# Kernel optimization log

Measured on AMD Instinct MI355X. Metric: run time of the kernel, lower is better.

## Reference

```python
import jax, jax.numpy as jnp
import numpy as np

N_NODES = 50000


def gcn_conv(x, W, b, src, dst, n_nodes):
    """PyG-style GCNConv: self-loops + symmetric deg^-1/2 normalization.

    x: [N, Fin], W: [Fin, Fout], b: [Fout], src/dst: [E] int.
    """
    h = x @ W  # [N, Fout] -- transform before aggregation (small GEMM)
    loop = jnp.arange(n_nodes, dtype=src.dtype)
    src2 = jnp.concatenate([src, loop])  # [E+N]
    dst2 = jnp.concatenate([dst, loop])
    # degree on target nodes (all edge weights = 1, includes self loops)
    deg = jax.ops.segment_sum(jnp.ones(src2.shape[0], dtype=h.dtype), dst2,
                              num_segments=n_nodes)
    dinv = jnp.where(deg > 0, jax.lax.rsqrt(deg), 0.0)
    norm = dinv[src2] * dinv[dst2]  # [E+N]
    msg = h[src2] * norm[:, None]   # gather + scale (memory bound)
    out = jax.ops.segment_sum(msg, dst2, num_segments=n_nodes)  # scatter-add
    return out + b


def setup_inputs() -> dict:
    key = jax.random.key(0)
    ks = jax.random.split(key, 8)
    input_dim, hidden_dim, output_dim = 128, 64, 64
    n_edges = 800000
    x = jax.random.normal(ks[0], (N_NODES, input_dim), dtype=jnp.float32)
    edge_index = jax.random.randint(ks[1], (2, n_edges), 0, N_NODES,
                                    dtype=jnp.int32)
    def glorot(k, fan_in, fan_out):
        s = jnp.sqrt(6.0 / (fan_in + fan_out)).astype(jnp.float32)
        return jax.random.uniform(k, (fan_in, fan_out), jnp.float32, -s, s)
    return {
        "x": x,
        "edge_index": edge_index,
        "W1": glorot(ks[2], input_dim, hidden_dim),
        "b1": jnp.zeros((hidden_dim,), jnp.float32),
        "W2": glorot(ks[3], hidden_dim, output_dim),
        "b2": jnp.zeros((output_dim,), jnp.float32),
        "Wfc": glorot(ks[4], output_dim, 1),
        "bfc": jnp.zeros((1,), jnp.float32),
    }


def reference(x, edge_index, W1, b1, W2, b2, Wfc, bfc):
    src, dst = edge_index[0], edge_index[1]
    h = gcn_conv(x, W1, b1, src, dst, N_NODES)
    h = jax.nn.relu(h)
    h = gcn_conv(h, W2, b2, src, dst, N_NODES)
    logits = h @ Wfc + bfc  # [N, 1]
    return jax.nn.sigmoid(logits)
```

## Files before the change

### kernel.cpp

```cpp
#include <hip/hip_runtime.h>
#include <hip/hip_bf16.h>

#define NN 50000
#define FIN 128
#define NT (NN / 16)
#define NREG 196
#define RCAP 5120
#define SLAB 8960

typedef unsigned short u16;
typedef unsigned int u32;
typedef __attribute__((ext_vector_type(8))) short short8;
typedef __attribute__((ext_vector_type(4))) float floatx4;

__device__ __forceinline__ float b2f(u16 v) {
  union { u32 u; float f; } x; x.u = ((u32)v) << 16; return x.f;
}
__device__ __forceinline__ u16 f2b(float f) {
  union { u32 u; float f; } x; x.f = f;
  u32 r = x.u + 0x7FFFu + ((x.u >> 16) & 1u);
  return (u16)(r >> 16);
}

__global__ __launch_bounds__(256) void k_prep_binA(
    const u32* __restrict__ xw, int nxw, const void* __restrict__ w1, int n1w,
    const void* __restrict__ w2, int n2w, const void* __restrict__ wf, int nfw,
    const u16* __restrict__ b2, const u16* __restrict__ bfc,
    u16* __restrict__ W1h, u16* __restrict__ W1l, float* __restrict__ w2f,
    float* __restrict__ cbias, int* __restrict__ flags,
    const int* __restrict__ src, const int* __restrict__ dst, int E,
    u32* __restrict__ bucket, int* __restrict__ gtail,
    u16* __restrict__ g, float* __restrict__ tvec) {
  int t = threadIdx.x;
  int blk = blockIdx.x;
  if (blk >= 33) {
    __shared__ int hist[NREG];
    __shared__ int base[NREG];
    for (int i = t; i < NREG; i += 256) hist[i] = 0;
    __syncthreads();
    int sl = blk - 33, nsl = 256;
    int lo = (int)((long long)sl * E / nsl);
    int hi = (int)((long long)(sl + 1) * E / nsl);
    for (int e = lo + t; e < hi; e += 256) atomicAdd(&hist[dst[e] >> 8], 1);
    __syncthreads();
    for (int i = t; i < NREG; i += 256) {
      int c = hist[i];
      base[i] = (c > 0) ? atomicAdd(&gtail[i], c) : 0;
      hist[i] = 0;
    }
    __syncthreads();
    for (int e = lo + t; e < hi; e += 256) {
      int d = dst[e];
      int r = d >> 8;
      int ofs = base[r] + atomicAdd(&hist[r], 1);
      if (ofs < RCAP)
        bucket[(size_t)r * RCAP + ofs] = ((u32)(d & 255) << 16) | (u32)src[e];
    }
    return;
  }
  __shared__ int sc[2];
  if (t < 2) sc[t] = 0;
  __syncthreads();
  if (blk < 32) {
    const u32* p = (const u32*)w1;
    int samples = n1w < 1024 ? n1w : 1024;
    int score = 0;
    for (int i = t; i < samples; i += 256) {
      u32 w = p[i];
      u32 e = (w >> 7) & 0xFFu;
      score += (e >= 100u && e <= 132u) ? 1 : -1;
    }
    if (score) atomicAdd(&sc[0], score);
    if (blk == 0) {
      int sn = nxw < 1024 ? nxw : 1024;
      int sx = 0;
      for (int i = t; i < sn; i += 256) {
        u32 w = xw[i];
        u32 e = (w >> 7) & 0xFFu;
        sx += (e >= 100u && e <= 132u) ? 1 : -1;
      }
      if (sx) atomicAdd(&sc[1], sx);
    }
    __syncthreads();
    int f1 = sc[0] > 0;
    if (blk == 0 && t == 0) {
      flags[0] = sc[1] > 0;
      flags[1] = f1;
    }
    int i = blk * 256 + t;
    int j = i & 7, L = (i >> 3) & 63, f = i >> 9;
    int k = (f >> 2) * 32 + (L >> 4) * 8 + j;
    int n = (f & 3) * 16 + (L & 15);
    int idx = k * 64 + n;
    float v = f1 ? b2f(((const u16*)w1)[idx]) : ((const float*)w1)[idx];
    u16 hb = f2b(v);
    W1h[i] = hb;
    W1l[i] = f2b(v - b2f(hb));
  } else {
    const u32* p2 = (const u32*)w2;
    const u32* pf = (const u32*)wf;
    int n2s = n2w < 1024 ? n2w : 1024;
    int nfs = nfw < 1024 ? nfw : 1024;
    int s2 = 0, sf = 0;
    for (int i = t; i < n2s; i += 256) {
      u32 w = p2[i];
      u32 e = (w >> 7) & 0xFFu;
      s2 += (e >= 100u && e <= 132u) ? 1 : -1;
    }
    for (int i = t; i < nfs; i += 256) {
      u32 w = pf[i];
      u32 e = (w >> 7) & 0xFFu;
      sf += (e >= 100u && e <= 132u) ? 1 : -1;
    }
    if (s2) atomicAdd(&sc[0], s2);
    if (sf) atomicAdd(&sc[1], sf);
    __syncthreads();
    int f2 = sc[0] > 0, f3 = sc[1] > 0;
    if (t == 0) { flags[2] = f2; flags[3] = f3; }
    if (t < 64) {
      float acc = 0.f;
      for (int j = 0; j < 64; ++j) {
        float w2v = f2 ? b2f(((const u16*)w2)[t * 64 + j])
                       : ((const float*)w2)[t * 64 + j];
        float wfv = f3 ? b2f(((const u16*)wf)[j]) : ((const float*)wf)[j];
        acc += w2v * wfv;
      }
      w2f[t] = acc;
    } else if (t == 64) {
      float acc = b2f(bfc[0]);
      for (int j = 0; j < 64; ++j) {
        float wfv = f3 ? b2f(((const u16*)wf)[j]) : ((const float*)wf)[j];
        acc += b2f(b2[j]) * wfv;
      }
      cbias[0] = acc;
    } else if (t >= 128 && t < 192) {
      g[(size_t)NN * 64 + (t - 128)] = 0;
    } else if (t == 192) {
      tvec[NN] = 0.f;
    }
  }
}

__global__ __launch_bounds__(256) void k_binB1(const u32* __restrict__ bucket,
                                               const int* __restrict__ gtail,
                                               int* __restrict__ cnt,
                                               int* __restrict__ rowstart,
                                               float* __restrict__ dinv) {
  __shared__ int h[256];
  __shared__ int smem[4];
  int r = blockIdx.x, t = threadIdx.x;
  h[t] = 0;
  __syncthreads();
  int n = gtail[r];
  if (n > RCAP) n = RCAP;
  const u32* b = bucket + (size_t)r * RCAP;
  for (int i = t; i < n; i += 256) atomicAdd(&h[b[i] >> 16], 1);
  __syncthreads();
  int v = r * 256 + t;
  int c = (v < NN) ? h[t] : 0;
  if (v < NN) {
    cnt[v] = c;
    dinv[v] = rsqrtf((float)(c + 1));
  }
  int p = (c + 15) & ~15;
  int lane = t & 63, w = t >> 6;
  int xv = p;
  for (int d = 1; d < 64; d <<= 1) {
    int y = __shfl_up(xv, d);
    if (lane >= d) xv += y;
  }
  if (lane == 63) smem[w] = xv;
  __syncthreads();
  int add = 0;
  for (int j = 0; j < w; ++j) add += smem[j];
  xv += add;
  if (v < NN) rowstart[v] = r * SLAB + xv - p;
}

__global__ __launch_bounds__(256) void k_gemm_scatter(
    const u32* __restrict__ bucket, const int* __restrict__ gtail,
    const int* __restrict__ rowstart, const int* __restrict__ cnt,
    u16* __restrict__ csr,
    const void* __restrict__ X, const u16* __restrict__ Wh,
    const u16* __restrict__ Wl, const float* __restrict__ dinv,
    u16* __restrict__ g, const int* __restrict__ flags) {
  int t = threadIdx.x;
  if (blockIdx.x < NREG) {
    __shared__ int off[256];
    int r = blockIdx.x;
    int v = r * 256 + t;
    int grs = (v < NN) ? rowstart[v] : 0;
    off[t] = grs;
    __syncthreads();
    int n = gtail[r];
    if (n > RCAP) n = RCAP;
    const u32* b = bucket + (size_t)r * RCAP;
    for (int i = t; i < n; i += 256) {
      u32 p = b[i];
      int pos = atomicAdd(&off[p >> 16], 1);
      csr[pos] = (u16)(p & 0xFFFFu);
    }
    __syncthreads();
    if (v < NN) {
      int end = grs + ((cnt[v] + 15) & ~15);
      for (int pos = off[t]; pos < end; ++pos) csr[pos] = (u16)NN;
    }
    return;
  }
  constexpr int KC = FIN / 32;
  int wave = t >> 6, lane = t & 63;
  int rt = (blockIdx.x - NREG) * 4 + wave;
  if (rt >= NT) return;
  int m = rt * 16 + (lane & 15);
  int q = (lane >> 4) * 8;
  bool xb = flags[0] != 0;

  short8 ah[KC], al[KC];
  if (xb) {
    const u16* xr = (const u16*)X + (size_t)m * FIN + q;
#pragma unroll
    for (int kc = 0; kc < KC; ++kc) ah[kc] = *(const short8*)(xr + kc * 32);
  } else {
    const float* xr = (const float*)X + (size_t)m * FIN + q;
#pragma unroll
    for (int kc = 0; kc < KC; ++kc) {
      float4 v0 = *(const float4*)(xr + kc * 32);
      float4 v1 = *(const float4*)(xr + kc * 32 + 4);
      float v[8] = {v0.x, v0.y, v0.z, v0.w, v1.x, v1.y, v1.z, v1.w};
      short8 h8, l8;
#pragma unroll
      for (int j = 0; j < 8; ++j) {
        u16 hb = f2b(v[j]);
        h8[j] = (short)hb;
        l8[j] = (short)f2b(v[j] - b2f(hb));
      }
      ah[kc] = h8;
      al[kc] = l8;
    }
  }

  int row0 = rt * 16 + (lane >> 4) * 4;
  int c0 = lane & 15;
  float dvr[4];
#pragma unroll
  for (int r = 0; r < 4; ++r) dvr[r] = dinv[row0 + r];
#pragma unroll
  for (int ct = 0; ct < 4; ++ct) {
    short8 bh[KC], bl[KC];
#pragma unroll
    for (int kc = 0; kc < KC; ++kc) {
      size_t fo = ((size_t)((kc * 4 + ct) * 64 + lane)) * 8;
      bh[kc] = *(const short8*)(Wh + fo);
      bl[kc] = *(const short8*)(Wl + fo);
    }
    floatx4 acc = (floatx4)(0.f);
#pragma unroll
    for (int kc = 0; kc < KC; ++kc) {
      if (!xb)
        acc = __builtin_amdgcn_mfma_f32_16x16x32_bf16(al[kc], bh[kc], acc, 0, 0, 0);
      acc = __builtin_amdgcn_mfma_f32_16x16x32_bf16(ah[kc], bl[kc], acc, 0, 0, 0);
      acc = __builtin_amdgcn_mfma_f32_16x16x32_bf16(ah[kc], bh[kc], acc, 0, 0, 0);
    }
    size_t o = (size_t)row0 * 64 + ct * 16 + c0;
#pragma unroll
    for (int r = 0; r < 4; ++r) g[o + (size_t)r * 64] = f2b(acc[r] * dvr[r]);
  }
}

__global__ __launch_bounds__(256) void k_agg1t(const u16* __restrict__ g,
                                               const float* __restrict__ dinv,
                                               const int* __restrict__ rowstart,
                                               const int* __restrict__ cnt,
                                               const u16* __restrict__ csr,
                                               const u16* __restrict__ bias,
                                               const float* __restrict__ w2f,
                                               float* __restrict__ tvec) {
  int tid = threadIdx.x;
  int wave = tid >> 6, lane = tid & 63;
  int v = (blockIdx.x * 4 + wave) * 4;
  int rs[4], pd[4];
  float dvl[4], acc[4];
  int pm = 0;
#pragma unroll
  for (int n = 0; n < 4; ++n) {
    rs[n] = rowstart[v + n];
    pd[n] = (cnt[v + n] + 15) & ~15;
    dvl[n] = dinv[v + n];
    acc[n] = b2f(g[(size_t)(v + n) * 64 + lane]);
    pm = pd[n] > pm ? pd[n] : pm;
  }
  for (int j = 0; j < pm; j += 16) {
    u32 cw[4][8];
    bool act[4];
#pragma unroll
    for (int n = 0; n < 4; ++n) {
      act[n] = j < pd[n];
      if (act[n]) {
        int b = rs[n] + j;
        uint4 c0 = *(const uint4*)(csr + b);
        uint4 c1 = *(const uint4*)(csr + b + 8);
        cw[n][0] = c0.x; cw[n][1] = c0.y; cw[n][2] = c0.z; cw[n][3] = c0.w;
        cw[n][4] = c1.x; cw[n][5] = c1.y; cw[n][6] = c1.z; cw[n][7] = c1.w;
      }
    }
    float hh[4][16];
#pragma unroll
    for (int n = 0; n < 4; ++n) {
      if (act[n]) {
#pragma unroll
        for (int i = 0; i < 8; ++i) {
          hh[n][2 * i] = b2f(g[(size_t)(cw[n][i] & 0xFFFFu) * 64 + lane]);
          hh[n][2 * i + 1] = b2f(g[(size_t)(cw[n][i] >> 16) * 64 + lane]);
        }
      }
    }
#pragma unroll
    for (int n = 0; n < 4; ++n) {
      if (act[n]) {
        float s0 = (hh[n][0] + hh[n][1]) + (hh[n][2] + hh[n][3]);
        float s1 = (hh[n][4] + hh[n][5]) + (hh[n][6] + hh[n][7]);
        float s2 = (hh[n][8] + hh[n][9]) + (hh[n][10] + hh[n][11]);
        float s3 = (hh[n][12] + hh[n][13]) + (hh[n][14] + hh[n][15]);
        acc[n] += (s0 + s1) + (s2 + s3);
      }
    }
  }
  float bv = b2f(bias[lane]);
  float wfv = w2f[lane];
  float val[4];
#pragma unroll
  for (int n = 0; n < 4; ++n) {
    val[n] = fmaxf(dvl[n] * acc[n] + bv, 0.0f) * wfv;
    for (int o = 32; o > 0; o >>= 1) val[n] += __shfl_xor(val[n], o);
  }
#pragma unroll
  for (int n = 0; n < 4; ++n)
    if (lane == n) tvec[v + n] = dvl[n] * val[n];
}

__global__ __launch_bounds__(256) void k_aggz(const float* __restrict__ tvec,
                                              const float* __restrict__ dinv,
                                              const int* __restrict__ rowstart,
                                              const int* __restrict__ cnt,
                                              const u16* __restrict__ csr,
                                              const float* __restrict__ cbias,
                                              void* __restrict__ out,
                                              const int* __restrict__ flags) {
  int tid = threadIdx.x;
  int wave = tid >> 6, lane = tid & 63;
  int sub = lane >> 4, slot = lane & 15;
  int v = blockIdx.x * 16 + wave * 4 + sub;
  int rs = rowstart[v];
  int pdeg = (cnt[v] + 15) & ~15;
  float acc = 0.f;
  for (int j = slot; j < pdeg; j += 16) acc += tvec[csr[rs + j]];
  for (int o = 8; o > 0; o >>= 1) acc += __shfl_xor(acc, o);
  if (slot == 0) {
    float dv = dinv[v];
    float z = dv * (acc + tvec[v]) + cbias[0];
    float sg = 1.0f / (1.0f + __expf(-z));
    if (flags[0]) ((u16*)out)[v] = f2b(sg);
    else ((float*)out)[v] = sg;
  }
}

extern "C" void kernel_launch(void* const* d_in, const int* in_sizes, int n_in,
                              void* d_out, int out_size, void* d_ws, size_t ws_size,
                              hipStream_t stream) {
  const void* x = d_in[0];
  const int* ei = (const int*)d_in[1];
  const void* W1 = d_in[2];
  const u16* b1 = (const u16*)d_in[3];
  const void* W2 = d_in[4];
  const u16* b2 = (const u16*)d_in[5];
  const void* Wfc = d_in[6];
  const u16* bfc = (const u16*)d_in[7];

  int E = in_sizes[1] / 2;
  const int* src = ei;
  const int* dst = ei + E;

  char* base = (char*)d_ws;
  size_t off = 0;
  auto alloc = [&](size_t bytes) {
    void* p = base + off;
    off = (off + bytes + 255) & ~(size_t)255;
    return p;
  };
  int* flags = (int*)alloc(8 * 4);
  u16* W1h = (u16*)alloc((size_t)FIN * 64 * 2);
  u16* W1l = (u16*)alloc((size_t)FIN * 64 * 2);
  float* w2f = (float*)alloc(64 * 4);
  float* cbias = (float*)alloc(4);
  int* cnt = (int*)alloc((size_t)NN * 4);
  int* rowstart = (int*)alloc((size_t)NN * 4);
  int* gtail = (int*)alloc((size_t)NREG * 4);
  u32* bucket = (u32*)alloc((size_t)NREG * RCAP * 4);
  u16* csr = (u16*)alloc((size_t)NREG * SLAB * 2);
  float* dinv = (float*)alloc((size_t)NN * 4);
  u16* g = (u16*)alloc((size_t)(NN + 1) * 64 * 2);
  float* tvec = (float*)alloc((size_t)(NN + 1) * 4);

  hipMemsetAsync(gtail, 0, (size_t)NREG * 4, stream);
  k_prep_binA<<<289, 256, 0, stream>>>(
      (const u32*)x, in_sizes[0] / 2, W1, in_sizes[2] / 2, W2, in_sizes[4] / 2,
      Wfc, in_sizes[6] / 2, b2, bfc, W1h, W1l, w2f, cbias, flags, src, dst, E,
      bucket, gtail, g, tvec);
  k_binB1<<<NREG, 256, 0, stream>>>(bucket, gtail, cnt, rowstart, dinv);
  k_gemm_scatter<<<NREG + (NT + 3) / 4, 256, 0, stream>>>(
      bucket, gtail, rowstart, cnt, csr, x, W1h, W1l, dinv, g, flags);
  k_agg1t<<<NN / 16, 256, 0, stream>>>(g, dinv, rowstart, cnt, csr, b1, w2f,
                                       tvec);
  k_aggz<<<NN / 16, 256, 0, stream>>>(tvec, dinv, rowstart, cnt, csr, cbias,
                                      d_out, flags);
}
```

Before: 159.6 us.

## Split layer-1 features into two 32-column halves, drop binB1 kernel, inline dinv

```diff
diff --git a/kernel.cpp b/kernel.cpp
--- a/kernel.cpp
+++ b/kernel.cpp
@@ -7,6 +7,7 @@
 #define NREG 196
 #define RCAP 5120
 #define SLAB 8960
+#define NB_AGG ((NN + 31) / 32)
 
 typedef unsigned short u16;
 typedef unsigned int u32;
@@ -29,8 +30,8 @@
     u16* __restrict__ W1h, u16* __restrict__ W1l, float* __restrict__ w2f,
     float* __restrict__ cbias, int* __restrict__ flags,
     const int* __restrict__ src, const int* __restrict__ dst, int E,
-    u32* __restrict__ bucket, int* __restrict__ gtail,
-    u16* __restrict__ g, float* __restrict__ tvec) {
+    u32* __restrict__ bucket, int* __restrict__ gtail, int* __restrict__ cnt,
+    u16* __restrict__ g0, u16* __restrict__ g1, float* __restrict__ tvec) {
   int t = threadIdx.x;
   int blk = blockIdx.x;
   if (blk >= 33) {
@@ -41,7 +42,11 @@
     int sl = blk - 33, nsl = 256;
     int lo = (int)((long long)sl * E / nsl);
     int hi = (int)((long long)(sl + 1) * E / nsl);
-    for (int e = lo + t; e < hi; e += 256) atomicAdd(&hist[dst[e] >> 8], 1);
+    for (int e = lo + t; e < hi; e += 256) {
+      int d = dst[e];
+      atomicAdd(&hist[d >> 8], 1);
+      atomicAdd(&cnt[d], 1);
+    }
     __syncthreads();
     for (int i = t; i < NREG; i += 256) {
       int c = hist[i];
@@ -133,76 +138,57 @@
         acc += b2f(b2[j]) * wfv;
       }
       cbias[0] = acc;
-    } else if (t >= 128 && t < 192) {
-      g[(size_t)NN * 64 + (t - 128)] = 0;
+    } else if (t >= 128 && t < 160) {
+      g0[(size_t)NN * 32 + (t - 128)] = 0;
+    } else if (t >= 160 && t < 192) {
+      g1[(size_t)NN * 32 + (t - 160)] = 0;
     } else if (t == 192) {
       tvec[NN] = 0.f;
     }
   }
 }
 
-__global__ __launch_bounds__(256) void k_binB1(const u32* __restrict__ bucket,
-                                               const int* __restrict__ gtail,
-                                               int* __restrict__ cnt,
-                                               int* __restrict__ rowstart,
-                                               float* __restrict__ dinv) {
-  __shared__ int h[256];
-  __shared__ int smem[4];
-  int r = blockIdx.x, t = threadIdx.x;
-  h[t] = 0;
-  __syncthreads();
-  int n = gtail[r];
-  if (n > RCAP) n = RCAP;
-  const u32* b = bucket + (size_t)r * RCAP;
-  for (int i = t; i < n; i += 256) atomicAdd(&h[b[i] >> 16], 1);
-  __syncthreads();
-  int v = r * 256 + t;
-  int c = (v < NN) ? h[t] : 0;
-  if (v < NN) {
-    cnt[v] = c;
-    dinv[v] = rsqrtf((float)(c + 1));
-  }
-  int p = (c + 15) & ~15;
-  int lane = t & 63, w = t >> 6;
-  int xv = p;
-  for (int d = 1; d < 64; d <<= 1) {
-    int y = __shfl_up(xv, d);
-    if (lane >= d) xv += y;
-  }
-  if (lane == 63) smem[w] = xv;
-  __syncthreads();
-  int add = 0;
-  for (int j = 0; j < w; ++j) add += smem[j];
-  xv += add;
-  if (v < NN) rowstart[v] = r * SLAB + xv - p;
-}
-
 __global__ __launch_bounds__(256) void k_gemm_scatter(
     const u32* __restrict__ bucket, const int* __restrict__ gtail,
-    const int* __restrict__ rowstart, const int* __restrict__ cnt,
+    int* __restrict__ rowstart, const int* __restrict__ cnt,
     u16* __restrict__ csr,
     const void* __restrict__ X, const u16* __restrict__ Wh,
-    const u16* __restrict__ Wl, const float* __restrict__ dinv,
-    u16* __restrict__ g, const int* __restrict__ flags) {
+    const u16* __restrict__ Wl, u16* __restrict__ g0, u16* __restrict__ g1,
+    const int* __restrict__ flags) {
   int t = threadIdx.x;
   if (blockIdx.x < NREG) {
     __shared__ int off[256];
+    __shared__ int sm4[4];
     int r = blockIdx.x;
     int v = r * 256 + t;
-    int grs = (v < NN) ? rowstart[v] : 0;
+    int c = (v < NN) ? cnt[v] : 0;
+    int p = (c + 15) & ~15;
+    int lane = t & 63, w = t >> 6;
+    int xv = p;
+    for (int d = 1; d < 64; d <<= 1) {
+      int y = __shfl_up(xv, d);
+      if (lane >= d) xv += y;
+    }
+    if (lane == 63) sm4[w] = xv;
+    __syncthreads();
+    int add = 0;
+    for (int j2 = 0; j2 < w; ++j2) add += sm4[j2];
+    xv += add;
+    int grs = r * SLAB + xv - p;
+    if (v < NN) rowstart[v] = grs;
     off[t] = grs;
     __syncthreads();
     int n = gtail[r];
     if (n > RCAP) n = RCAP;
     const u32* b = bucket + (size_t)r * RCAP;
     for (int i = t; i < n; i += 256) {
-      u32 p = b[i];
-      int pos = atomicAdd(&off[p >> 16], 1);
-      csr[pos] = (u16)(p & 0xFFFFu);
+      u32 pk = b[i];
+      int pos = atomicAdd(&off[pk >> 16], 1);
+      csr[pos] = (u16)(pk & 0xFFFFu);
     }
     __syncthreads();
     if (v < NN) {
-      int end = grs + ((cnt[v] + 15) & ~15);
+      int end = grs + p;
       for (int pos = off[t]; pos < end; ++pos) csr[pos] = (u16)NN;
     }
     return;
@@ -243,7 +229,8 @@
   int c0 = lane & 15;
   float dvr[4];
 #pragma unroll
-  for (int r = 0; r < 4; ++r) dvr[r] = dinv[row0 + r];
+  for (int r = 0; r < 4; ++r)
+    dvr[r] = rsqrtf((float)(cnt[row0 + r] + 1));
 #pragma unroll
   for (int ct = 0; ct < 4; ++ct) {
     short8 bh[KC], bl[KC];
@@ -261,32 +248,43 @@
       acc = __builtin_amdgcn_mfma_f32_16x16x32_bf16(ah[kc], bl[kc], acc, 0, 0, 0);
       acc = __builtin_amdgcn_mfma_f32_16x16x32_bf16(ah[kc], bh[kc], acc, 0, 0, 0);
     }
-    size_t o = (size_t)row0 * 64 + ct * 16 + c0;
-#pragma unroll
-    for (int r = 0; r < 4; ++r) g[o + (size_t)r * 64] = f2b(acc[r] * dvr[r]);
-  }
-}
-
-__global__ __launch_bounds__(256) void k_agg1t(const u16* __restrict__ g,
-                                               const float* __restrict__ dinv,
+#pragma unroll
+    for (int r = 0; r < 4; ++r) {
+      u16 ov = f2b(acc[r] * dvr[r]);
+      if (ct < 2)
+        g0[(size_t)(row0 + r) * 32 + ct * 16 + c0] = ov;
+      else
+        g1[(size_t)(row0 + r) * 32 + (ct - 2) * 16 + c0] = ov;
+    }
+  }
+}
+
+__global__ __launch_bounds__(256) void k_agg1p(const u16* __restrict__ gp,
                                                const int* __restrict__ rowstart,
                                                const int* __restrict__ cnt,
                                                const u16* __restrict__ csr,
                                                const u16* __restrict__ bias,
                                                const float* __restrict__ w2f,
-                                               float* __restrict__ tvec) {
+                                               float* __restrict__ tvec,
+                                               int pass) {
   int tid = threadIdx.x;
   int wave = tid >> 6, lane = tid & 63;
-  int v = (blockIdx.x * 4 + wave) * 4;
+  int h = lane >> 5, col = lane & 31;
+  int vb = (blockIdx.x * 4 + wave) * 8 + h * 4;
   int rs[4], pd[4];
   float dvl[4], acc[4];
+  bool ok[4];
   int pm = 0;
 #pragma unroll
   for (int n = 0; n < 4; ++n) {
-    rs[n] = rowstart[v + n];
-    pd[n] = (cnt[v + n] + 15) & ~15;
-    dvl[n] = dinv[v + n];
-    acc[n] = b2f(g[(size_t)(v + n) * 64 + lane]);
+    int nv = vb + n;
+    ok[n] = nv < NN;
+    int cv = ok[n] ? nv : 0;
+    int c = ok[n] ? cnt[cv] : 0;
+    rs[n] = rowstart[cv];
+    pd[n] = ok[n] ? ((c + 15) & ~15) : 0;
+    dvl[n] = rsqrtf((float)(c + 1));
+    acc[n] = ok[n] ? b2f(gp[(size_t)cv * 32 + col]) : 0.f;
     pm = pd[n] > pm ? pd[n] : pm;
   }
   for (int j = 0; j < pm; j += 16) {
@@ -297,10 +295,10 @@
       act[n] = j < pd[n];
       if (act[n]) {
         int b = rs[n] + j;
-        uint4 c0 = *(const uint4*)(csr + b);
-        uint4 c1 = *(const uint4*)(csr + b + 8);
-        cw[n][0] = c0.x; cw[n][1] = c0.y; cw[n][2] = c0.z; cw[n][3] = c0.w;
-        cw[n][4] = c1.x; cw[n][5] = c1.y; cw[n][6] = c1.z; cw[n][7] = c1.w;
+        uint4 uq0 = *(const uint4*)(csr + b);
+        uint4 uq1 = *(const uint4*)(csr + b + 8);
+        cw[n][0] = uq0.x; cw[n][1] = uq0.y; cw[n][2] = uq0.z; cw[n][3] = uq0.w;
+        cw[n][4] = uq1.x; cw[n][5] = uq1.y; cw[n][6] = uq1.z; cw[n][7] = uq1.w;
       }
     }
     float hh[4][16];
@@ -309,8 +307,8 @@
       if (act[n]) {
 #pragma unroll
         for (int i = 0; i < 8; ++i) {
-          hh[n][2 * i] = b2f(g[(size_t)(cw[n][i] & 0xFFFFu) * 64 + lane]);
-          hh[n][2 * i + 1] = b2f(g[(size_t)(cw[n][i] >> 16) * 64 + lane]);
+          hh[n][2 * i] = b2f(gp[(size_t)(cw[n][i] & 0xFFFFu) * 32 + col]);
+          hh[n][2 * i + 1] = b2f(gp[(size_t)(cw[n][i] >> 16) * 32 + col]);
         }
       }
     }
@@ -325,21 +323,22 @@
       }
     }
   }
-  float bv = b2f(bias[lane]);
-  float wfv = w2f[lane];
-  float val[4];
+  int c = col + pass * 32;
+  float bv = b2f(bias[c]);
+  float wfv = w2f[c];
 #pragma unroll
   for (int n = 0; n < 4; ++n) {
-    val[n] = fmaxf(dvl[n] * acc[n] + bv, 0.0f) * wfv;
-    for (int o = 32; o > 0; o >>= 1) val[n] += __shfl_xor(val[n], o);
-  }
-#pragma unroll
-  for (int n = 0; n < 4; ++n)
-    if (lane == n) tvec[v + n] = dvl[n] * val[n];
+    float val = fmaxf(dvl[n] * acc[n] + bv, 0.0f) * wfv;
+    for (int o = 16; o > 0; o >>= 1) val += __shfl_xor(val, o);
+    if (col == n && ok[n]) {
+      int nv = vb + n;
+      float rr = dvl[n] * val;
+      tvec[nv] = pass ? (tvec[nv] + rr) : rr;
+    }
+  }
 }
 
 __global__ __launch_bounds__(256) void k_aggz(const float* __restrict__ tvec,
-                                              const float* __restrict__ dinv,
                                               const int* __restrict__ rowstart,
                                               const int* __restrict__ cnt,
                                               const u16* __restrict__ csr,
@@ -351,12 +350,13 @@
   int sub = lane >> 4, slot = lane & 15;
   int v = blockIdx.x * 16 + wave * 4 + sub;
   int rs = rowstart[v];
-  int pdeg = (cnt[v] + 15) & ~15;
+  int cv = cnt[v];
+  int pdeg = (cv + 15) & ~15;
   float acc = 0.f;
   for (int j = slot; j < pdeg; j += 16) acc += tvec[csr[rs + j]];
   for (int o = 8; o > 0; o >>= 1) acc += __shfl_xor(acc, o);
   if (slot == 0) {
-    float dv = dinv[v];
+    float dv = rsqrtf((float)(cv + 1));
     float z = dv * (acc + tvec[v]) + cbias[0];
     float sg = 1.0f / (1.0f + __expf(-z));
     if (flags[0]) ((u16*)out)[v] = f2b(sg);
@@ -392,25 +392,25 @@
   u16* W1l = (u16*)alloc((size_t)FIN * 64 * 2);
   float* w2f = (float*)alloc(64 * 4);
   float* cbias = (float*)alloc(4);
-  int* cnt = (int*)alloc((size_t)NN * 4);
   int* rowstart = (int*)alloc((size_t)NN * 4);
   int* gtail = (int*)alloc((size_t)NREG * 4);
+  int* cnt = (int*)alloc((size_t)NN * 4);
   u32* bucket = (u32*)alloc((size_t)NREG * RCAP * 4);
   u16* csr = (u16*)alloc((size_t)NREG * SLAB * 2);
-  float* dinv = (float*)alloc((size_t)NN * 4);
-  u16* g = (u16*)alloc((size_t)(NN + 1) * 64 * 2);
+  u16* g0 = (u16*)alloc((size_t)(NN + 1) * 32 * 2);
+  u16* g1 = (u16*)alloc((size_t)(NN + 1) * 32 * 2);
   float* tvec = (float*)alloc((size_t)(NN + 1) * 4);
 
-  hipMemsetAsync(gtail, 0, (size_t)NREG * 4, stream);
+  size_t zbytes = (size_t)((char*)(cnt + NN) - (char*)gtail);
+  hipMemsetAsync(gtail, 0, zbytes, stream);
   k_prep_binA<<<289, 256, 0, stream>>>(
       (const u32*)x, in_sizes[0] / 2, W1, in_sizes[2] / 2, W2, in_sizes[4] / 2,
       Wfc, in_sizes[6] / 2, b2, bfc, W1h, W1l, w2f, cbias, flags, src, dst, E,
-      bucket, gtail, g, tvec);
-  k_binB1<<<NREG, 256, 0, stream>>>(bucket, gtail, cnt, rowstart, dinv);
+      bucket, gtail, cnt, g0, g1, tvec);
   k_gemm_scatter<<<NREG + (NT + 3) / 4, 256, 0, stream>>>(
-      bucket, gtail, rowstart, cnt, csr, x, W1h, W1l, dinv, g, flags);
-  k_agg1t<<<NN / 16, 256, 0, stream>>>(g, dinv, rowstart, cnt, csr, b1, w2f,
-                                       tvec);
-  k_aggz<<<NN / 16, 256, 0, stream>>>(tvec, dinv, rowstart, cnt, csr, cbias,
-                                      d_out, flags);
-}
+      bucket, gtail, rowstart, cnt, csr, x, W1h, W1l, g0, g1, flags);
+  k_agg1p<<<NB_AGG, 256, 0, stream>>>(g0, rowstart, cnt, csr, b1, w2f, tvec, 0);
+  k_agg1p<<<NB_AGG, 256, 0, stream>>>(g1, rowstart, cnt, csr, b1, w2f, tvec, 1);
+  k_aggz<<<NN / 16, 256, 0, stream>>>(tvec, rowstart, cnt, csr, cbias, d_out,
+                                      flags);
+}
```

Measured after the change: 193.1 us. 1.21x slower.

## Build CSR via global atomic degree count and direct scatter, dropping bucket pass

Applied to the files above, without the earlier changes.

```diff
diff --git a/kernel.cpp b/kernel.cpp
--- a/kernel.cpp
+++ b/kernel.cpp
@@ -5,8 +5,10 @@
 #define FIN 128
 #define NT (NN / 16)
 #define NREG 196
-#define RCAP 5120
 #define SLAB 8960
+#define NSLH 512
+#define NSLS 512
+#define NGEMB ((NT + 3) / 4)
 
 typedef unsigned short u16;
 typedef unsigned int u32;
@@ -22,40 +24,21 @@
   return (u16)(r >> 16);
 }
 
-__global__ __launch_bounds__(256) void k_prep_binA(
+__global__ __launch_bounds__(256) void k_prep_hist(
     const u32* __restrict__ xw, int nxw, const void* __restrict__ w1, int n1w,
     const void* __restrict__ w2, int n2w, const void* __restrict__ wf, int nfw,
     const u16* __restrict__ b2, const u16* __restrict__ bfc,
     u16* __restrict__ W1h, u16* __restrict__ W1l, float* __restrict__ w2f,
     float* __restrict__ cbias, int* __restrict__ flags,
-    const int* __restrict__ src, const int* __restrict__ dst, int E,
-    u32* __restrict__ bucket, int* __restrict__ gtail,
+    const int* __restrict__ dst, int E, int* __restrict__ cnt,
     u16* __restrict__ g, float* __restrict__ tvec) {
   int t = threadIdx.x;
   int blk = blockIdx.x;
   if (blk >= 33) {
-    __shared__ int hist[NREG];
-    __shared__ int base[NREG];
-    for (int i = t; i < NREG; i += 256) hist[i] = 0;
-    __syncthreads();
-    int sl = blk - 33, nsl = 256;
-    int lo = (int)((long long)sl * E / nsl);
-    int hi = (int)((long long)(sl + 1) * E / nsl);
-    for (int e = lo + t; e < hi; e += 256) atomicAdd(&hist[dst[e] >> 8], 1);
-    __syncthreads();
-    for (int i = t; i < NREG; i += 256) {
-      int c = hist[i];
-      base[i] = (c > 0) ? atomicAdd(&gtail[i], c) : 0;
-      hist[i] = 0;
-    }
-    __syncthreads();
-    for (int e = lo + t; e < hi; e += 256) {
-      int d = dst[e];
-      int r = d >> 8;
-      int ofs = base[r] + atomicAdd(&hist[r], 1);
-      if (ofs < RCAP)
-        bucket[(size_t)r * RCAP + ofs] = ((u32)(d & 255) << 16) | (u32)src[e];
-    }
+    int sl = blk - 33;
+    int lo = (int)((long long)sl * E / NSLH);
+    int hi = (int)((long long)(sl + 1) * E / NSLH);
+    for (int e = lo + t; e < hi; e += 256) atomicAdd(&cnt[dst[e]], 1);
     return;
   }
   __shared__ int sc[2];
@@ -141,27 +124,14 @@
   }
 }
 
-__global__ __launch_bounds__(256) void k_binB1(const u32* __restrict__ bucket,
-                                               const int* __restrict__ gtail,
-                                               int* __restrict__ cnt,
-                                               int* __restrict__ rowstart,
-                                               float* __restrict__ dinv) {
-  __shared__ int h[256];
-  __shared__ int smem[4];
+__global__ __launch_bounds__(256) void k_scan(const int* __restrict__ cnt,
+                                              int* __restrict__ rowstart,
+                                              int* __restrict__ wo,
+                                              u16* __restrict__ csr) {
+  __shared__ int sm4[4];
   int r = blockIdx.x, t = threadIdx.x;
-  h[t] = 0;
-  __syncthreads();
-  int n = gtail[r];
-  if (n > RCAP) n = RCAP;
-  const u32* b = bucket + (size_t)r * RCAP;
-  for (int i = t; i < n; i += 256) atomicAdd(&h[b[i] >> 16], 1);
-  __syncthreads();
   int v = r * 256 + t;
-  int c = (v < NN) ? h[t] : 0;
-  if (v < NN) {
-    cnt[v] = c;
-    dinv[v] = rsqrtf((float)(c + 1));
-  }
+  int c = (v < NN) ? cnt[v] : 0;
   int p = (c + 15) & ~15;
   int lane = t & 63, w = t >> 6;
   int xv = p;
@@ -169,47 +139,41 @@
     int y = __shfl_up(xv, d);
     if (lane >= d) xv += y;
   }
-  if (lane == 63) smem[w] = xv;
+  if (lane == 63) sm4[w] = xv;
   __syncthreads();
   int add = 0;
-  for (int j = 0; j < w; ++j) add += smem[j];
+  for (int j = 0; j < w; ++j) add += sm4[j];
   xv += add;
-  if (v < NN) rowstart[v] = r * SLAB + xv - p;
+  int grs = r * SLAB + xv - p;
+  if (v < NN) {
+    rowstart[v] = grs;
+    wo[v] = grs;
+    for (int pos = grs + c; pos < grs + p; ++pos) csr[pos] = (u16)NN;
+  }
 }
 
 __global__ __launch_bounds__(256) void k_gemm_scatter(
-    const u32* __restrict__ bucket, const int* __restrict__ gtail,
-    const int* __restrict__ rowstart, const int* __restrict__ cnt,
-    u16* __restrict__ csr,
+    const int* __restrict__ src, const int* __restrict__ dst, int E,
+    int* __restrict__ wo, u16* __restrict__ csr,
     const void* __restrict__ X, const u16* __restrict__ Wh,
-    const u16* __restrict__ Wl, const float* __restrict__ dinv,
+    const u16* __restrict__ Wl, const int* __restrict__ cnt,
     u16* __restrict__ g, const int* __restrict__ flags) {
   int t = threadIdx.x;
-  if (blockIdx.x < NREG) {
-    __shared__ int off[256];
-    int r = blockIdx.x;
-    int v = r * 256 + t;
-    int grs = (v < NN) ? rowstart[v] : 0;
-    off[t] = grs;
-    __syncthreads();
-    int n = gtail[r];
-    if (n > RCAP) n = RCAP;
-    const u32* b = bucket + (size_t)r * RCAP;
-    for (int i = t; i < n; i += 256) {
-      u32 p = b[i];
-      int pos = atomicAdd(&off[p >> 16], 1);
-      csr[pos] = (u16)(p & 0xFFFFu);
-    }
-    __syncthreads();
-    if (v < NN) {
-      int end = grs + ((cnt[v] + 15) & ~15);
-      for (int pos = off[t]; pos < end; ++pos) csr[pos] = (u16)NN;
+  if (blockIdx.x >= NGEMB) {
+    int sl = blockIdx.x - NGEMB;
+    int lo = (int)((long long)sl * E / NSLS);
+    int hi = (int)((long long)(sl + 1) * E / NSLS);
+    for (int e = lo + t; e < hi; e += 256) {
+      int d = dst[e];
+      int s = src[e];
+      int pos = atomicAdd(&wo[d], 1);
+      csr[pos] = (u16)s;
     }
     return;
   }
   constexpr int KC = FIN / 32;
   int wave = t >> 6, lane = t & 63;
-  int rt = (blockIdx.x - NREG) * 4 + wave;
+  int rt = blockIdx.x * 4 + wave;
   if (rt >= NT) return;
   int m = rt * 16 + (lane & 15);
   int q = (lane >> 4) * 8;
@@ -243,7 +207,8 @@
   int c0 = lane & 15;
   float dvr[4];
 #pragma unroll
-  for (int r = 0; r < 4; ++r) dvr[r] = dinv[row0 + r];
+  for (int r = 0; r < 4; ++r)
+    dvr[r] = rsqrtf((float)(cnt[row0 + r] + 1));
 #pragma unroll
   for (int ct = 0; ct < 4; ++ct) {
     short8 bh[KC], bl[KC];
@@ -268,9 +233,8 @@
 }
 
 __global__ __launch_bounds__(256) void k_agg1t(const u16* __restrict__ g,
-                                               const float* __restrict__ dinv,
+                                               const int* __restrict__ cnt,
                                                const int* __restrict__ rowstart,
-                                               const int* __restrict__ cnt,
                                                const u16* __restrict__ csr,
                                                const u16* __restrict__ bias,
                                                const float* __restrict__ w2f,
@@ -284,8 +248,9 @@
 #pragma unroll
   for (int n = 0; n < 4; ++n) {
     rs[n] = rowstart[v + n];
-    pd[n] = (cnt[v + n] + 15) & ~15;
-    dvl[n] = dinv[v + n];
+    int c = cnt[v + n];
+    pd[n] = (c + 15) & ~15;
+    dvl[n] = rsqrtf((float)(c + 1));
     acc[n] = b2f(g[(size_t)(v + n) * 64 + lane]);
     pm = pd[n] > pm ? pd[n] : pm;
   }
@@ -339,7 +304,6 @@
 }
 
 __global__ __launch_bounds__(256) void k_aggz(const float* __restrict__ tvec,
-                                              const float* __restrict__ dinv,
                                               const int* __restrict__ rowstart,
                                               const int* __restrict__ cnt,
                                               const u16* __restrict__ csr,
@@ -351,12 +315,13 @@
   int sub = lane >> 4, slot = lane & 15;
   int v = blockIdx.x * 16 + wave * 4 + sub;
   int rs = rowstart[v];
-  int pdeg = (cnt[v] + 15) & ~15;
+  int cv = cnt[v];
+  int pdeg = (cv + 15) & ~15;
   float acc = 0.f;
   for (int j = slot; j < pdeg; j += 16) acc += tvec[csr[rs + j]];
   for (int o = 8; o > 0; o >>= 1) acc += __shfl_xor(acc, o);
   if (slot == 0) {
-    float dv = dinv[v];
+    float dv = rsqrtf((float)(cv + 1));
     float z = dv * (acc + tvec[v]) + cbias[0];
     float sg = 1.0f / (1.0f + __expf(-z));
     if (flags[0]) ((u16*)out)[v] = f2b(sg);
@@ -394,23 +359,20 @@
   float* cbias = (float*)alloc(4);
   int* cnt = (int*)alloc((size_t)NN * 4);
   int* rowstart = (int*)alloc((size_t)NN * 4);
-  int* gtail = (int*)alloc((size_t)NREG * 4);
-  u32* bucket = (u32*)alloc((size_t)NREG * RCAP * 4);
+  int* wo = (int*)alloc((size_t)NN * 4);
   u16* csr = (u16*)alloc((size_t)NREG * SLAB * 2);
-  float* dinv = (float*)alloc((size_t)NN * 4);
   u16* g = (u16*)alloc((size_t)(NN + 1) * 64 * 2);
   float* tvec = (float*)alloc((size_t)(NN + 1) * 4);
 
-  hipMemsetAsync(gtail, 0, (size_t)NREG * 4, stream);
-  k_prep_binA<<<289, 256, 0, stream>>>(
+  hipMemsetAsync(cnt, 0, (size_t)NN * 4, stream);
+  k_prep_hist<<<33 + NSLH, 256, 0, stream>>>(
       (const u32*)x, in_sizes[0] / 2, W1, in_sizes[2] / 2, W2, in_sizes[4] / 2,
-      Wfc, in_sizes[6] / 2, b2, bfc, W1h, W1l, w2f, cbias, flags, src, dst, E,
-      bucket, gtail, g, tvec);
-  k_binB1<<<NREG, 256, 0, stream>>>(bucket, gtail, cnt, rowstart, dinv);
-  k_gemm_scatter<<<NREG + (NT + 3) / 4, 256, 0, stream>>>(
-      bucket, gtail, rowstart, cnt, csr, x, W1h, W1l, dinv, g, flags);
-  k_agg1t<<<NN / 16, 256, 0, stream>>>(g, dinv, rowstart, cnt, csr, b1, w2f,
-                                       tvec);
-  k_aggz<<<NN / 16, 256, 0, stream>>>(tvec, dinv, rowstart, cnt, csr, cbias,
-                                      d_out, flags);
-}
+      Wfc, in_sizes[6] / 2, b2, bfc, W1h, W1l, w2f, cbias, flags, dst, E, cnt,
+      g, tvec);
+  k_scan<<<NREG, 256, 0, stream>>>(cnt, rowstart, wo, csr);
+  k_gemm_scatter<<<NGEMB + NSLS, 256, 0, stream>>>(src, dst, E, wo, csr, x,
+                                                   W1h, W1l, cnt, g, flags);
+  k_agg1t<<<NN / 16, 256, 0, stream>>>(g, cnt, rowstart, csr, b1, w2f, tvec);
+  k_aggz<<<NN / 16, 256, 0, stream>>>(tvec, rowstart, cnt, csr, cbias, d_out,
+                                      flags);
+}
```

After: 205.9 us. +29.0%, slower.
